# Optimization experiments

Measured on AMD Instinct MI355X. Metric: run time of the kernel, lower is better.

Reference implementation:

```python
import jax, jax.numpy as jnp
import numpy as np

N, E, D_IN, D_OUT = 50000, 800000, 128, 128
LN_EPS = 1e-5


def setup_inputs() -> dict:
    key = jax.random.key(0)
    ks = jax.random.split(key, 7)
    x = jax.random.normal(ks[0], (N, D_IN), dtype=jnp.float32)
    adj = jax.random.randint(ks[1], (2, E), 0, N, dtype=jnp.int32)  # edge_index
    scale = 1.0 / np.sqrt(D_IN)
    W_gcn = jax.random.normal(ks[2], (D_IN, D_OUT), dtype=jnp.float32) * scale
    b_gcn = jax.random.normal(ks[3], (D_OUT,), dtype=jnp.float32) * 0.02
    W_lin = jax.random.normal(ks[4], (D_IN, D_OUT), dtype=jnp.float32) * scale
    ln_w = jnp.ones((D_OUT,), dtype=jnp.float32)
    ln_b = jnp.zeros((D_OUT,), dtype=jnp.float32)
    return {"adj": adj, "x": x, "W_gcn": W_gcn, "b_gcn": b_gcn,
            "W_lin": W_lin, "ln_w": ln_w, "ln_b": ln_b}


def _gcn_conv(x, edge_index, W, b):
    """PyG GCNConv: add self-loops, symmetric D^-1/2 (A+I) D^-1/2 normalization."""
    n = x.shape[0]
    loop = jnp.arange(n, dtype=edge_index.dtype)
    src = jnp.concatenate([edge_index[0], loop])  # message sources (x_j)
    dst = jnp.concatenate([edge_index[1], loop])  # aggregation targets
    ones = jnp.ones(src.shape[0], dtype=x.dtype)
    deg = jax.ops.segment_sum(ones, dst, num_segments=n)
    dinv = jnp.where(deg > 0, jax.lax.rsqrt(deg), 0.0)
    norm = dinv[src] * dinv[dst]                   # [E+N]
    h = x @ W                                      # [N, D_OUT] project first (PyG order)
    msg = h[src] * norm[:, None]                   # gather + scale
    agg = jax.ops.segment_sum(msg, dst, num_segments=n)
    return agg + b


def _layer_norm(y, w, b):
    mu = jnp.mean(y, axis=-1, keepdims=True)
    var = jnp.mean(jnp.square(y - mu), axis=-1, keepdims=True)
    return (y - mu) * jax.lax.rsqrt(var + LN_EPS) * w + b


def reference(adj, x, W_gcn, b_gcn, W_lin, ln_w, ln_b):
    x1 = _gcn_conv(x, adj, W_gcn, b_gcn)
    x2 = x @ W_lin                                  # bias=False linear
    return _layer_norm(x1 + x2 + 1e-6, ln_w, ln_b)
```

## Files before the change

kernel.cpp:

```cpp
#include <hip/hip_runtime.h>
#include <hip/hip_bf16.h>

#define NN 50000
#define EE 800000
#define DD 128
#define CB 196
#define NFB 1563
#define EBLK 2048
#define NEBK 391
#define HST 392

typedef __attribute__((ext_vector_type(8))) short bf16x8;
typedef __attribute__((ext_vector_type(4))) float f32x4;

static __device__ __forceinline__ unsigned short f2bf(float f) {
  union { float f; unsigned u; } v; v.f = f;
  unsigned r = v.u + 0x7FFFu + ((v.u >> 16) & 1u);
  return (unsigned short)(r >> 16);
}
static __device__ __forceinline__ float bf2f(unsigned short h) {
  union { unsigned u; float f; } v; v.u = ((unsigned)h) << 16;
  return v.f;
}

__global__ __launch_bounds__(256) void k_p0(
    const int* __restrict__ dst, int* __restrict__ hist,
    const float* __restrict__ Wg, const float* __restrict__ Wl,
    unsigned short* __restrict__ Wt, const float4* __restrict__ x4,
    ushort4* __restrict__ xb4) {
  int b = blockIdx.x, t = threadIdx.x;
  if (b < NEBK) {
    __shared__ int cnt[CB];
    for (int i = t; i < CB; i += 256) cnt[i] = 0;
    __syncthreads();
    int e0 = b * EBLK;
    for (int i = t; i < EBLK; i += 256) {
      int e = e0 + i;
      if (e < EE) atomicAdd(&cnt[dst[e] >> 8], 1);
    }
    __syncthreads();
    if (t < CB) {
      hist[t * HST + b] = cnt[t];
      if (b == 0) hist[t * HST + (HST - 1)] = 0;
    }
  } else if (b < NEBK + 32) {
    for (int i = (b - NEBK) * 256 + t; i < DD * 256; i += 32 * 256) {
      int n = i >> 8, k = i & 255;
      float v = (k < 128) ? Wg[k * DD + n] : Wl[(k - 128) * DD + n];
      Wt[i] = f2bf(v);
    }
  } else {
    int base = (b - NEBK - 32) * 1024 + t;
#pragma unroll
    for (int k = 0; k < 4; k++) {
      int i = base + k * 256;
      if (i < NN * 32) {
        float4 v = x4[i];
        ushort4 o;
        o.x = f2bf(v.x); o.y = f2bf(v.y); o.z = f2bf(v.z); o.w = f2bf(v.w);
        xb4[i] = o;
      }
    }
  }
}

__global__ __launch_bounds__(512) void k_scatter(
    const int* __restrict__ src, const int* __restrict__ dst,
    const int* __restrict__ hist, int* __restrict__ bucketBase,
    int* __restrict__ bucketTot, unsigned int* __restrict__ pairs) {
  __shared__ unsigned int rec[EBLK];
  __shared__ unsigned int sorted[EBLK];
  __shared__ int sTo[2][CB], sCh[2][CB], sOw[2][CB];
  __shared__ unsigned int sc[256];
  __shared__ int cur[CB], gofs[CB];
  int blk = blockIdx.x, t = threadIdx.x;
  int e0 = blk * EBLK;
  int vcnt = EE - e0; if (vcnt > EBLK) vcnt = EBLK;
  for (int i = t; i < vcnt; i += 512) {
    int d = dst[e0 + i], s = src[e0 + i];
    rec[i] = (unsigned int)s | ((unsigned int)(d & 255) << 16) |
             ((unsigned int)(d >> 8) << 24);
  }
  int q = t & 255, h = t >> 8;
  if (q < CB) {
    const uint4* hp = (const uint4*)(hist + (size_t)q * HST + h * (HST / 2));
    int cb0 = h * (HST / 2);
    int to = 0, ch = 0, ow = 0;
#pragma unroll 7
    for (int v = 0; v < HST / 8; ++v) {
      uint4 hv = hp[v];
      int c = cb0 + v * 4;
      int a0 = (int)hv.x, a1 = (int)hv.y, a2 = (int)hv.z, a3 = (int)hv.w;
      to += a0 + a1 + a2 + a3;
      ch += (c + 0 < blk ? a0 : 0) + (c + 1 < blk ? a1 : 0) +
            (c + 2 < blk ? a2 : 0) + (c + 3 < blk ? a3 : 0);
      ow += (c + 0 == blk ? a0 : 0) + (c + 1 == blk ? a1 : 0) +
            (c + 2 == blk ? a2 : 0) + (c + 3 == blk ? a3 : 0);
    }
    sTo[h][q] = to; sCh[h][q] = ch; sOw[h][q] = ow;
  }
  __syncthreads();
  int totv = 0, chpv = 0, ownv = 0;
  if (t < CB) {
    totv = sTo[0][t] + sTo[1][t];
    chpv = sCh[0][t] + sCh[1][t];
    ownv = sOw[0][t] + sOw[1][t];
  }
  if (t < 256) sc[t] = (t < CB) ? (((unsigned)totv << 12) | (unsigned)ownv) : 0u;
  for (int off = 1; off < 256; off <<= 1) {
    __syncthreads();
    unsigned tmp = (t < 256 && t >= off) ? sc[t - off] : 0u;
    __syncthreads();
    if (t < 256 && t >= off) sc[t] += tmp;
  }
  __syncthreads();
  if (t < CB) {
    unsigned v = sc[t];
    int incT = (int)(v >> 12), incO = (int)(v & 4095u);
    int gb = incT - totv;
    int lo = incO - ownv;
    cur[t] = lo;
    gofs[t] = gb + chpv - lo;
    if (blk == 0) { bucketBase[t] = gb; bucketTot[t] = totv; }
  }
  __syncthreads();
  for (int i = t; i < vcnt; i += 512) {
    unsigned int r = rec[i];
    int p = atomicAdd(&cur[r >> 24], 1);
    sorted[p] = r;
  }
  __syncthreads();
  for (int i = t; i < vcnt; i += 512) {
    unsigned int r = sorted[i];
    pairs[gofs[r >> 24] + i] = r;
  }
}

__global__ __launch_bounds__(512) void k_p1b(
    const unsigned int* __restrict__ pairs, const int* __restrict__ bucketBase,
    const int* __restrict__ bucketTot, const unsigned short* __restrict__ xb,
    int* __restrict__ deg, float* __restrict__ dinv, int* __restrict__ rowStart,
    unsigned short* __restrict__ srcU16, unsigned short* __restrict__ xs) {
  __shared__ int ldeg[256], lscan[256], lcur[256];
  __shared__ float ldinvs[256];
  int b = blockIdx.x, t = threadIdx.x;
  int n0 = b << 8;
  int nloc = NN - n0; if (nloc > 256) nloc = 256;
  int start = bucketBase[b];
  int cnt = bucketTot[b];
  if (t < 256) ldeg[t] = 0;
  __syncthreads();
  for (int i = t; i < cnt; i += 512)
    atomicAdd(&ldeg[(pairs[start + i] >> 16) & 255], 1);
  __syncthreads();
  int dg = (t < 256) ? ldeg[t] : 0;
  if (t < 256) lscan[t] = dg;
  for (int off = 1; off < 256; off <<= 1) {
    __syncthreads();
    int tmp = (t < 256 && t >= off) ? lscan[t - off] : 0;
    __syncthreads();
    if (t < 256 && t >= off) lscan[t] += tmp;
  }
  __syncthreads();
  if (t < 256) {
    int rs = start + lscan[t] - dg;
    lcur[t] = rs;
    float di = rsqrtf((float)(dg + 1));
    ldinvs[t] = di;
    if (t < nloc) { deg[n0 + t] = dg; dinv[n0 + t] = di; rowStart[n0 + t] = rs; }
  }
  __syncthreads();
  for (int i = t; i < cnt; i += 512) {
    unsigned int pr = pairs[start + i];
    int pos = atomicAdd(&lcur[(pr >> 16) & 255], 1);
    srcU16[pos] = (unsigned short)(pr & 0xFFFFu);
  }
  for (int i = t; i < nloc * 16; i += 512) {
    int rr = i >> 4, qq = i & 15;
    bf16x8 v = *(const bf16x8*)(xb + (size_t)(n0 + rr) * DD + qq * 8);
    float di = ldinvs[rr];
    bf16x8 o;
#pragma unroll
    for (int k = 0; k < 8; k++) o[k] = (short)f2bf(bf2f((unsigned short)v[k]) * di);
    *(bf16x8*)(xs + (size_t)(n0 + rr) * DD + qq * 8) = o;
  }
}

static __device__ __forceinline__ void gather16(
    const unsigned short* __restrict__ xs, const unsigned short* __restrict__ srcU16,
    int js, int cnt, int r, int srcLaneBase, float* acc) {
  for (int base = 0; base < cnt; base += 16) {
    int idx = (base + r < cnt) ? (int)srcU16[js + base + r] : 0;
    int m = cnt - base; if (m > 16) m = 16;
    int j = 0;
    for (; j + 8 <= m; j += 8) {
      int s0 = __shfl(idx, srcLaneBase + j);
      int s1 = __shfl(idx, srcLaneBase + j + 1);
      int s2 = __shfl(idx, srcLaneBase + j + 2);
      int s3 = __shfl(idx, srcLaneBase + j + 3);
      int s4 = __shfl(idx, srcLaneBase + j + 4);
      int s5 = __shfl(idx, srcLaneBase + j + 5);
      int s6 = __shfl(idx, srcLaneBase + j + 6);
      int s7 = __shfl(idx, srcLaneBase + j + 7);
      bf16x8 v0 = *(const bf16x8*)(xs + (size_t)s0 * DD + r * 8);
      bf16x8 v1 = *(const bf16x8*)(xs + (size_t)s1 * DD + r * 8);
      bf16x8 v2 = *(const bf16x8*)(xs + (size_t)s2 * DD + r * 8);
      bf16x8 v3 = *(const bf16x8*)(xs + (size_t)s3 * DD + r * 8);
      bf16x8 v4 = *(const bf16x8*)(xs + (size_t)s4 * DD + r * 8);
      bf16x8 v5 = *(const bf16x8*)(xs + (size_t)s5 * DD + r * 8);
      bf16x8 v6 = *(const bf16x8*)(xs + (size_t)s6 * DD + r * 8);
      bf16x8 v7 = *(const bf16x8*)(xs + (size_t)s7 * DD + r * 8);
#pragma unroll
      for (int k = 0; k < 8; k++) acc[k] += bf2f((unsigned short)v0[k]);
#pragma unroll
      for (int k = 0; k < 8; k++) acc[k] += bf2f((unsigned short)v1[k]);
#pragma unroll
      for (int k = 0; k < 8; k++) acc[k] += bf2f((unsigned short)v2[k]);
#pragma unroll
      for (int k = 0; k < 8; k++) acc[k] += bf2f((unsigned short)v3[k]);
#pragma unroll
      for (int k = 0; k < 8; k++) acc[k] += bf2f((unsigned short)v4[k]);
#pragma unroll
      for (int k = 0; k < 8; k++) acc[k] += bf2f((unsigned short)v5[k]);
#pragma unroll
      for (int k = 0; k < 8; k++) acc[k] += bf2f((unsigned short)v6[k]);
#pragma unroll
      for (int k = 0; k < 8; k++) acc[k] += bf2f((unsigned short)v7[k]);
    }
    for (; j < m; j++) {
      int s = __shfl(idx, srcLaneBase + j);
      bf16x8 v = *(const bf16x8*)(xs + (size_t)s * DD + r * 8);
#pragma unroll
      for (int k = 0; k < 8; k++) acc[k] += bf2f((unsigned short)v[k]);
    }
  }
}

__global__ __launch_bounds__(512) void k_mega4(
    const unsigned short* __restrict__ xs, const unsigned short* __restrict__ xb,
    const int* __restrict__ rowStart, const int* __restrict__ deg,
    const unsigned short* __restrict__ srcU16, const float* __restrict__ dinv,
    const unsigned short* __restrict__ Wt, const float* __restrict__ bgcn,
    const float* __restrict__ lnw, const float* __restrict__ lnb,
    float* __restrict__ out) {
  __shared__ unsigned short abuf[32 * 136];
  int b = blockIdx.x, t = threadIdx.x;
  int n0 = b * 32;
  int g = t >> 4, r = t & 15;
  int lane = t & 63;
  int srcLaneBase = lane & 48;
  int node = n0 + g;
  bool valid = (node < NN);
  int nc = valid ? node : (NN - 1);
  float acc[8];
  {
    bf16x8 va = *(const bf16x8*)(xs + (size_t)nc * DD + r * 8);
#pragma unroll
    for (int k = 0; k < 8; k++) acc[k] = bf2f((unsigned short)va[k]);
  }
  int js = valid ? rowStart[nc] : 0;
  int cnt = valid ? deg[nc] : 0;
  gather16(xs, srcU16, js, cnt, r, srcLaneBase, acc);
  {
    float d = dinv[nc];
    bf16x8 o;
#pragma unroll
    for (int k = 0; k < 8; k++) o[k] = valid ? (short)f2bf(acc[k] * d) : (short)0;
    *(bf16x8*)&abuf[g * 136 + r * 8] = o;
  }
  __syncthreads();
  if (t < 128) {
    int w = t >> 6, lane2 = t & 63;
    int quad = lane2 >> 4, rr = lane2 & 15;
    int mloc = w * 16 + rr;
    int rowA = n0 + mloc; int rc = (rowA < NN) ? rowA : (NN - 1);
    f32x4 zero = {0.f, 0.f, 0.f, 0.f};
    f32x4 macc[8];
#pragma unroll
    for (int i = 0; i < 8; i++) macc[i] = zero;
#pragma unroll
    for (int ks = 0; ks < 8; ks++) {
      bf16x8 a;
      if (ks < 4) a = *(const bf16x8*)&abuf[mloc * 136 + ks * 32 + quad * 8];
      else        a = *(const bf16x8*)(xb + (size_t)rc * DD + (ks - 4) * 32 + quad * 8);
#pragma unroll
      for (int nt = 0; nt < 8; nt++) {
        bf16x8 bb = *(const bf16x8*)(Wt + (size_t)(nt * 16 + rr) * 256 + ks * 32 + quad * 8);
        macc[nt] = __builtin_amdgcn_mfma_f32_16x16x32_bf16(a, bb, macc[nt], 0, 0, 0);
      }
    }
    float bg[8], lw[8], lb[8];
#pragma unroll
    for (int nt = 0; nt < 8; nt++) {
      int col = nt * 16 + rr;
      bg[nt] = bgcn[col] + 1e-6f;
      lw[nt] = lnw[col];
      lb[nt] = lnb[col];
    }
#pragma unroll
    for (int reg = 0; reg < 4; reg++) {
      float y[8];
      float s1 = 0.f, s2 = 0.f;
#pragma unroll
      for (int nt = 0; nt < 8; nt++) {
        y[nt] = macc[nt][reg] + bg[nt];
        s1 += y[nt];
        s2 += y[nt] * y[nt];
      }
#pragma unroll
      for (int off = 1; off < 16; off <<= 1) {
        s1 += __shfl_xor(s1, off);
        s2 += __shfl_xor(s2, off);
      }
      float mu = s1 * (1.0f / 128.0f);
      float var = s2 * (1.0f / 128.0f) - mu * mu;
      float inv = rsqrtf(var + 1e-5f);
      int row = n0 + w * 16 + quad * 4 + reg;
      if (row < NN) {
#pragma unroll
        for (int nt = 0; nt < 8; nt++) {
          out[(size_t)row * DD + nt * 16 + rr] = (y[nt] - mu) * inv * lw[nt] + lb[nt];
        }
      }
    }
  }
}

extern "C" void kernel_launch(void* const* d_in, const int* in_sizes, int n_in,
                              void* d_out, int out_size, void* d_ws, size_t ws_size,
                              hipStream_t stream) {
  const int* adj = (const int*)d_in[0];
  const float* x = (const float*)d_in[1];
  const float* Wg = (const float*)d_in[2];
  const float* bg = (const float*)d_in[3];
  const float* Wl = (const float*)d_in[4];
  const float* lw = (const float*)d_in[5];
  const float* lb = (const float*)d_in[6];
  const int* srcp = adj;
  const int* dstp = adj + EE;
  float* out = (float*)d_out;

  char* ws = (char*)d_ws;
  size_t off = 0;
  auto alloc = [&](size_t bytes) -> void* {
    void* p = ws + off;
    off += (bytes + 255) & ~(size_t)255;
    return p;
  };
  int* hist = (int*)alloc((size_t)CB * HST * 4);
  int* bucketBase = (int*)alloc((size_t)256 * 4);
  int* bucketTot = (int*)alloc((size_t)256 * 4);
  unsigned int* pairs = (unsigned int*)alloc((size_t)EE * 4);
  unsigned short* srcU16 = (unsigned short*)alloc((size_t)EE * 2);
  int* deg = (int*)alloc((size_t)NN * 4);
  float* dinv = (float*)alloc((size_t)NN * 4);
  int* rowStart = (int*)alloc((size_t)NN * 4);
  unsigned short* xb = (unsigned short*)alloc((size_t)NN * DD * 2);
  unsigned short* xs = (unsigned short*)alloc((size_t)NN * DD * 2);
  unsigned short* Wt = (unsigned short*)alloc((size_t)DD * 256 * 2);
  (void)ws_size; (void)in_sizes; (void)n_in; (void)out_size;

  k_p0<<<NEBK + 32 + 1563, 256, 0, stream>>>(dstp, hist, Wg, Wl, Wt,
                                             (const float4*)x, (ushort4*)xb);
  k_scatter<<<NEBK, 512, 0, stream>>>(srcp, dstp, hist, bucketBase, bucketTot,
                                      pairs);
  k_p1b<<<CB, 512, 0, stream>>>(pairs, bucketBase, bucketTot, xb, deg, dinv,
                                rowStart, srcU16, xs);
  k_mega4<<<NFB, 512, 0, stream>>>(xs, xb, rowStart, deg, srcU16, dinv, Wt,
                                   bg, lw, lb, out);
}
```

Baseline: 187.1 us.

## Fuse preprocessing kernels into one cooperative kernel with grid syncs

Replaces the histogram, scatter and CSR-build kernels with a single cooperative kernel of 256 blocks that uses grid.sync between phases, and changes edge chunks from 2048 to 3125 per block. The aim is to remove two kernel launch boundaries and their tail effects. The scaled-x conversion now runs over the whole grid instead of only the 196 bucket blocks. In exchange, only 256 blocks are in flight during the bandwidth-bound x conversion, and each grid barrier adds its own cost.

```diff
diff --git a/kernel.cpp b/kernel.cpp
--- a/kernel.cpp
+++ b/kernel.cpp
@@ -1,4 +1,5 @@
 #include <hip/hip_runtime.h>
+#include <hip/hip_cooperative_groups.h>
 #include <hip/hip_bf16.h>
 
 #define NN 50000
@@ -6,12 +7,14 @@
 #define DD 128
 #define CB 196
 #define NFB 1563
-#define EBLK 2048
-#define NEBK 391
-#define HST 392
+#define GB 256
+#define GT 512
+#define ECH 3125
 
 typedef __attribute__((ext_vector_type(8))) short bf16x8;
 typedef __attribute__((ext_vector_type(4))) float f32x4;
+
+namespace cg = cooperative_groups;
 
 static __device__ __forceinline__ unsigned short f2bf(float f) {
   union { float f; unsigned u; } v; v.f = f;
@@ -23,88 +26,86 @@
   return v.f;
 }
 
-__global__ __launch_bounds__(256) void k_p0(
-    const int* __restrict__ dst, int* __restrict__ hist,
-    const float* __restrict__ Wg, const float* __restrict__ Wl,
-    unsigned short* __restrict__ Wt, const float4* __restrict__ x4,
-    ushort4* __restrict__ xb4) {
-  int b = blockIdx.x, t = threadIdx.x;
-  if (b < NEBK) {
-    __shared__ int cnt[CB];
-    for (int i = t; i < CB; i += 256) cnt[i] = 0;
-    __syncthreads();
-    int e0 = b * EBLK;
-    for (int i = t; i < EBLK; i += 256) {
-      int e = e0 + i;
-      if (e < EE) atomicAdd(&cnt[dst[e] >> 8], 1);
-    }
-    __syncthreads();
-    if (t < CB) {
-      hist[t * HST + b] = cnt[t];
-      if (b == 0) hist[t * HST + (HST - 1)] = 0;
-    }
-  } else if (b < NEBK + 32) {
-    for (int i = (b - NEBK) * 256 + t; i < DD * 256; i += 32 * 256) {
+__global__ __launch_bounds__(GT) void k_fused(
+    const int* __restrict__ src, const int* __restrict__ dst,
+    const float* __restrict__ x, const float* __restrict__ Wg,
+    const float* __restrict__ Wl, int* __restrict__ hist,
+    int* __restrict__ bucketBase, int* __restrict__ bucketTot,
+    unsigned int* __restrict__ pairs, unsigned short* __restrict__ srcU16,
+    int* __restrict__ deg, float* __restrict__ dinv,
+    int* __restrict__ rowStart, unsigned short* __restrict__ Wt,
+    unsigned short* __restrict__ xb, unsigned short* __restrict__ xs) {
+  __shared__ unsigned int smem[8320];
+  cg::grid_group grid = cg::this_grid();
+  int blk = blockIdx.x, t = threadIdx.x;
+
+  unsigned int* rec = smem;
+  int* cnt = (int*)(smem + 6272);
+  for (int i = t; i < CB; i += GT) cnt[i] = 0;
+  __syncthreads();
+  int e0 = blk * ECH;
+  for (int i = t; i < ECH; i += GT) {
+    int d = dst[e0 + i], s = src[e0 + i];
+    rec[i] = (unsigned)s | ((unsigned)(d & 255) << 16) |
+             ((unsigned)(d >> 8) << 24);
+    atomicAdd(&cnt[d >> 8], 1);
+  }
+  {
+    int i = blk * GT + t;
+    if (i < DD * 256) {
       int n = i >> 8, k = i & 255;
       float v = (k < 128) ? Wg[k * DD + n] : Wl[(k - 128) * DD + n];
       Wt[i] = f2bf(v);
     }
-  } else {
-    int base = (b - NEBK - 32) * 1024 + t;
-#pragma unroll
-    for (int k = 0; k < 4; k++) {
-      int i = base + k * 256;
-      if (i < NN * 32) {
-        float4 v = x4[i];
-        ushort4 o;
-        o.x = f2bf(v.x); o.y = f2bf(v.y); o.z = f2bf(v.z); o.w = f2bf(v.w);
-        xb4[i] = o;
-      }
-    }
-  }
-}
-
-__global__ __launch_bounds__(512) void k_scatter(
-    const int* __restrict__ src, const int* __restrict__ dst,
-    const int* __restrict__ hist, int* __restrict__ bucketBase,
-    int* __restrict__ bucketTot, unsigned int* __restrict__ pairs) {
-  __shared__ unsigned int rec[EBLK];
-  __shared__ unsigned int sorted[EBLK];
-  __shared__ int sTo[2][CB], sCh[2][CB], sOw[2][CB];
-  __shared__ unsigned int sc[256];
-  __shared__ int cur[CB], gofs[CB];
-  int blk = blockIdx.x, t = threadIdx.x;
-  int e0 = blk * EBLK;
-  int vcnt = EE - e0; if (vcnt > EBLK) vcnt = EBLK;
-  for (int i = t; i < vcnt; i += 512) {
-    int d = dst[e0 + i], s = src[e0 + i];
-    rec[i] = (unsigned int)s | ((unsigned int)(d & 255) << 16) |
-             ((unsigned int)(d >> 8) << 24);
-  }
-  int q = t & 255, h = t >> 8;
-  if (q < CB) {
-    const uint4* hp = (const uint4*)(hist + (size_t)q * HST + h * (HST / 2));
-    int cb0 = h * (HST / 2);
-    int to = 0, ch = 0, ow = 0;
-#pragma unroll 7
-    for (int v = 0; v < HST / 8; ++v) {
-      uint4 hv = hp[v];
-      int c = cb0 + v * 4;
-      int a0 = (int)hv.x, a1 = (int)hv.y, a2 = (int)hv.z, a3 = (int)hv.w;
-      to += a0 + a1 + a2 + a3;
-      ch += (c + 0 < blk ? a0 : 0) + (c + 1 < blk ? a1 : 0) +
-            (c + 2 < blk ? a2 : 0) + (c + 3 < blk ? a3 : 0);
-      ow += (c + 0 == blk ? a0 : 0) + (c + 1 == blk ? a1 : 0) +
-            (c + 2 == blk ? a2 : 0) + (c + 3 == blk ? a3 : 0);
-    }
-    sTo[h][q] = to; sCh[h][q] = ch; sOw[h][q] = ow;
+  }
+  {
+    const float4* x4 = (const float4*)x;
+    ushort4* xb4 = (ushort4*)xb;
+    for (int i = blk * GT + t; i < NN * 32; i += GB * GT) {
+      float4 v = x4[i];
+      ushort4 o;
+      o.x = f2bf(v.x); o.y = f2bf(v.y); o.z = f2bf(v.z); o.w = f2bf(v.w);
+      xb4[i] = o;
+    }
+  }
+  __syncthreads();
+  for (int i = t; i < CB; i += GT) hist[i * GB + blk] = cnt[i];
+  __threadfence();
+  grid.sync();
+
+  unsigned int* sorted = smem + 3136;
+  int* sTo = (int*)(smem + 6272);
+  int* sCh = (int*)(smem + 6664);
+  int* sOw = (int*)(smem + 7056);
+  unsigned int* sc = smem + 7448;
+  int* cur = (int*)(smem + 7704);
+  int* gofs = (int*)(smem + 7900);
+  {
+    int q = t & 255, h = t >> 8;
+    if (q < CB) {
+      const uint4* hp = (const uint4*)(hist + q * GB + h * 128);
+      int c0 = h * 128;
+      int to = 0, ch = 0, ow = 0;
+#pragma unroll 8
+      for (int v = 0; v < 32; ++v) {
+        uint4 hv = hp[v];
+        int c = c0 + v * 4;
+        int a0 = (int)hv.x, a1 = (int)hv.y, a2 = (int)hv.z, a3 = (int)hv.w;
+        to += a0 + a1 + a2 + a3;
+        ch += (c + 0 < blk ? a0 : 0) + (c + 1 < blk ? a1 : 0) +
+              (c + 2 < blk ? a2 : 0) + (c + 3 < blk ? a3 : 0);
+        ow += (c + 0 == blk ? a0 : 0) + (c + 1 == blk ? a1 : 0) +
+              (c + 2 == blk ? a2 : 0) + (c + 3 == blk ? a3 : 0);
+      }
+      sTo[h * CB + q] = to; sCh[h * CB + q] = ch; sOw[h * CB + q] = ow;
+    }
   }
   __syncthreads();
   int totv = 0, chpv = 0, ownv = 0;
   if (t < CB) {
-    totv = sTo[0][t] + sTo[1][t];
-    chpv = sCh[0][t] + sCh[1][t];
-    ownv = sOw[0][t] + sOw[1][t];
+    totv = sTo[t] + sTo[CB + t];
+    chpv = sCh[t] + sCh[CB + t];
+    ownv = sOw[t] + sOw[CB + t];
   }
   if (t < 256) sc[t] = (t < CB) ? (((unsigned)totv << 12) | (unsigned)ownv) : 0u;
   for (int off = 1; off < 256; off <<= 1) {
@@ -116,73 +117,74 @@
   __syncthreads();
   if (t < CB) {
     unsigned v = sc[t];
-    int incT = (int)(v >> 12), incO = (int)(v & 4095u);
-    int gb = incT - totv;
-    int lo = incO - ownv;
+    int gb = (int)(v >> 12) - totv;
+    int lo = (int)(v & 4095u) - ownv;
     cur[t] = lo;
     gofs[t] = gb + chpv - lo;
     if (blk == 0) { bucketBase[t] = gb; bucketTot[t] = totv; }
   }
   __syncthreads();
-  for (int i = t; i < vcnt; i += 512) {
-    unsigned int r = rec[i];
+  for (int i = t; i < ECH; i += GT) {
+    unsigned r = rec[i];
     int p = atomicAdd(&cur[r >> 24], 1);
     sorted[p] = r;
   }
   __syncthreads();
-  for (int i = t; i < vcnt; i += 512) {
-    unsigned int r = sorted[i];
+  for (int i = t; i < ECH; i += GT) {
+    unsigned r = sorted[i];
     pairs[gofs[r >> 24] + i] = r;
   }
-}
-
-__global__ __launch_bounds__(512) void k_p1b(
-    const unsigned int* __restrict__ pairs, const int* __restrict__ bucketBase,
-    const int* __restrict__ bucketTot, const unsigned short* __restrict__ xb,
-    int* __restrict__ deg, float* __restrict__ dinv, int* __restrict__ rowStart,
-    unsigned short* __restrict__ srcU16, unsigned short* __restrict__ xs) {
-  __shared__ int ldeg[256], lscan[256], lcur[256];
-  __shared__ float ldinvs[256];
-  int b = blockIdx.x, t = threadIdx.x;
-  int n0 = b << 8;
-  int nloc = NN - n0; if (nloc > 256) nloc = 256;
-  int start = bucketBase[b];
-  int cnt = bucketTot[b];
-  if (t < 256) ldeg[t] = 0;
-  __syncthreads();
-  for (int i = t; i < cnt; i += 512)
-    atomicAdd(&ldeg[(pairs[start + i] >> 16) & 255], 1);
-  __syncthreads();
-  int dg = (t < 256) ? ldeg[t] : 0;
-  if (t < 256) lscan[t] = dg;
-  for (int off = 1; off < 256; off <<= 1) {
-    __syncthreads();
-    int tmp = (t < 256 && t >= off) ? lscan[t - off] : 0;
-    __syncthreads();
-    if (t < 256 && t >= off) lscan[t] += tmp;
-  }
-  __syncthreads();
-  if (t < 256) {
-    int rs = start + lscan[t] - dg;
-    lcur[t] = rs;
-    float di = rsqrtf((float)(dg + 1));
-    ldinvs[t] = di;
-    if (t < nloc) { deg[n0 + t] = dg; dinv[n0 + t] = di; rowStart[n0 + t] = rs; }
-  }
-  __syncthreads();
-  for (int i = t; i < cnt; i += 512) {
-    unsigned int pr = pairs[start + i];
-    int pos = atomicAdd(&lcur[(pr >> 16) & 255], 1);
-    srcU16[pos] = (unsigned short)(pr & 0xFFFFu);
-  }
-  for (int i = t; i < nloc * 16; i += 512) {
-    int rr = i >> 4, qq = i & 15;
-    bf16x8 v = *(const bf16x8*)(xb + (size_t)(n0 + rr) * DD + qq * 8);
-    float di = ldinvs[rr];
+  __threadfence();
+  grid.sync();
+
+  int* ldeg = (int*)smem;
+  int* lscan = (int*)smem + 256;
+  int* lcur = (int*)smem + 512;
+  if (blk < CB) {
+    int n0 = blk << 8;
+    int nloc = NN - n0; if (nloc > 256) nloc = 256;
+    int start = bucketBase[blk], cntb = bucketTot[blk];
+    if (t < 256) ldeg[t] = 0;
+    __syncthreads();
+    for (int i = t; i < cntb; i += GT)
+      atomicAdd(&ldeg[(pairs[start + i] >> 16) & 255], 1);
+    __syncthreads();
+    int dg = (t < 256) ? ldeg[t] : 0;
+    if (t < 256) lscan[t] = dg;
+    for (int off = 1; off < 256; off <<= 1) {
+      __syncthreads();
+      int tmp = (t < 256 && t >= off) ? lscan[t - off] : 0;
+      __syncthreads();
+      if (t < 256 && t >= off) lscan[t] += tmp;
+    }
+    __syncthreads();
+    if (t < 256) {
+      int rs = start + lscan[t] - dg;
+      lcur[t] = rs;
+      if (t < nloc) {
+        deg[n0 + t] = dg;
+        dinv[n0 + t] = rsqrtf((float)(dg + 1));
+        rowStart[n0 + t] = rs;
+      }
+    }
+    __syncthreads();
+    for (int i = t; i < cntb; i += GT) {
+      unsigned pr = pairs[start + i];
+      int pos = atomicAdd(&lcur[(pr >> 16) & 255], 1);
+      srcU16[pos] = (unsigned short)(pr & 0xFFFFu);
+    }
+  }
+  __threadfence();
+  grid.sync();
+
+  for (int i = blk * GT + t; i < NN * 16; i += GB * GT) {
+    int row = i >> 4;
+    float di = dinv[row];
+    bf16x8 v = *(const bf16x8*)(xb + (size_t)i * 8);
     bf16x8 o;
 #pragma unroll
     for (int k = 0; k < 8; k++) o[k] = (short)f2bf(bf2f((unsigned short)v[k]) * di);
-    *(bf16x8*)(xs + (size_t)(n0 + rr) * DD + qq * 8) = o;
+    *(bf16x8*)(xs + (size_t)i * 8) = o;
   }
 }
 
@@ -347,7 +349,7 @@
     off += (bytes + 255) & ~(size_t)255;
     return p;
   };
-  int* hist = (int*)alloc((size_t)CB * HST * 4);
+  int* hist = (int*)alloc((size_t)CB * GB * 4);
   int* bucketBase = (int*)alloc((size_t)256 * 4);
   int* bucketTot = (int*)alloc((size_t)256 * 4);
   unsigned int* pairs = (unsigned int*)alloc((size_t)EE * 4);
@@ -360,12 +362,13 @@
   unsigned short* Wt = (unsigned short*)alloc((size_t)DD * 256 * 2);
   (void)ws_size; (void)in_sizes; (void)n_in; (void)out_size;
 
-  k_p0<<<NEBK + 32 + 1563, 256, 0, stream>>>(dstp, hist, Wg, Wl, Wt,
-                                             (const float4*)x, (ushort4*)xb);
-  k_scatter<<<NEBK, 512, 0, stream>>>(srcp, dstp, hist, bucketBase, bucketTot,
-                                      pairs);
-  k_p1b<<<CB, 512, 0, stream>>>(pairs, bucketBase, bucketTot, xb, deg, dinv,
-                                rowStart, srcU16, xs);
+  void* args[] = {(void*)&srcp, (void*)&dstp, (void*)&x, (void*)&Wg,
+                  (void*)&Wl, (void*)&hist, (void*)&bucketBase,
+                  (void*)&bucketTot, (void*)&pairs, (void*)&srcU16,
+                  (void*)&deg, (void*)&dinv, (void*)&rowStart, (void*)&Wt,
+                  (void*)&xb, (void*)&xs};
+  hipLaunchCooperativeKernel((const void*)k_fused, dim3(GB), dim3(GT), args, 0,
+                             stream);
   k_mega4<<<NFB, 512, 0, stream>>>(xs, xb, rowStart, deg, srcU16, dinv, Wt,
                                    bg, lw, lb, out);
 }
```

Result: slower. 422.7 us (+125.9%).

## Split fused GEMM+LayerNorm epilogue across all 8 waves with LDS row-stat reduction

Applied to the files above, without the earlier changes.

Previously only 2 of 8 waves ran the MFMA GEMM and LayerNorm epilogue while the other 6 sat idle. Now every wave computes a 16-row by 32-column tile, so the per-wave MFMA chain and register use shrink. Row sums for LayerNorm are combined across the four column-pair waves through shared memory. This costs an extra barrier and more total loads of A from LDS and xb.

```diff
diff --git a/kernel.cpp b/kernel.cpp
--- a/kernel.cpp
+++ b/kernel.cpp
@@ -236,7 +236,7 @@
   }
 }
 
-__global__ __launch_bounds__(512) void k_mega4(
+__global__ __launch_bounds__(512) void k_mega5(
     const unsigned short* __restrict__ xs, const unsigned short* __restrict__ xb,
     const int* __restrict__ rowStart, const int* __restrict__ deg,
     const unsigned short* __restrict__ srcU16, const float* __restrict__ dinv,
@@ -244,6 +244,7 @@
     const float* __restrict__ lnw, const float* __restrict__ lnb,
     float* __restrict__ out) {
   __shared__ unsigned short abuf[32 * 136];
+  __shared__ float lnred[4][32][2];
   int b = blockIdx.x, t = threadIdx.x;
   int n0 = b * 32;
   int g = t >> 4, r = t & 15;
@@ -269,58 +270,68 @@
     *(bf16x8*)&abuf[g * 136 + r * 8] = o;
   }
   __syncthreads();
-  if (t < 128) {
-    int w = t >> 6, lane2 = t & 63;
-    int quad = lane2 >> 4, rr = lane2 & 15;
-    int mloc = w * 16 + rr;
-    int rowA = n0 + mloc; int rc = (rowA < NN) ? rowA : (NN - 1);
-    f32x4 zero = {0.f, 0.f, 0.f, 0.f};
-    f32x4 macc[8];
-#pragma unroll
-    for (int i = 0; i < 8; i++) macc[i] = zero;
-#pragma unroll
-    for (int ks = 0; ks < 8; ks++) {
-      bf16x8 a;
-      if (ks < 4) a = *(const bf16x8*)&abuf[mloc * 136 + ks * 32 + quad * 8];
-      else        a = *(const bf16x8*)(xb + (size_t)rc * DD + (ks - 4) * 32 + quad * 8);
-#pragma unroll
-      for (int nt = 0; nt < 8; nt++) {
-        bf16x8 bb = *(const bf16x8*)(Wt + (size_t)(nt * 16 + rr) * 256 + ks * 32 + quad * 8);
-        macc[nt] = __builtin_amdgcn_mfma_f32_16x16x32_bf16(a, bb, macc[nt], 0, 0, 0);
-      }
-    }
-    float bg[8], lw[8], lb[8];
-#pragma unroll
-    for (int nt = 0; nt < 8; nt++) {
-      int col = nt * 16 + rr;
-      bg[nt] = bgcn[col] + 1e-6f;
-      lw[nt] = lnw[col];
-      lb[nt] = lnb[col];
-    }
-#pragma unroll
-    for (int reg = 0; reg < 4; reg++) {
-      float y[8];
-      float s1 = 0.f, s2 = 0.f;
-#pragma unroll
-      for (int nt = 0; nt < 8; nt++) {
-        y[nt] = macc[nt][reg] + bg[nt];
-        s1 += y[nt];
-        s2 += y[nt] * y[nt];
-      }
-#pragma unroll
-      for (int off = 1; off < 16; off <<= 1) {
-        s1 += __shfl_xor(s1, off);
-        s2 += __shfl_xor(s2, off);
-      }
-      float mu = s1 * (1.0f / 128.0f);
-      float var = s2 * (1.0f / 128.0f) - mu * mu;
-      float inv = rsqrtf(var + 1e-5f);
-      int row = n0 + w * 16 + quad * 4 + reg;
-      if (row < NN) {
-#pragma unroll
-        for (int nt = 0; nt < 8; nt++) {
-          out[(size_t)row * DD + nt * 16 + rr] = (y[nt] - mu) * inv * lw[nt] + lb[nt];
-        }
+  int w = t >> 6, lane2 = t & 63;
+  int quad = lane2 >> 4, rr = lane2 & 15;
+  int rowTile = w & 1, colPair = w >> 1;
+  int mloc = rowTile * 16 + rr;
+  int rowA = n0 + mloc; int rc = (rowA < NN) ? rowA : (NN - 1);
+  f32x4 zero = {0.f, 0.f, 0.f, 0.f};
+  f32x4 macc[2];
+  macc[0] = zero; macc[1] = zero;
+#pragma unroll
+  for (int ks = 0; ks < 8; ks++) {
+    bf16x8 a;
+    if (ks < 4) a = *(const bf16x8*)&abuf[mloc * 136 + ks * 32 + quad * 8];
+    else        a = *(const bf16x8*)(xb + (size_t)rc * DD + (ks - 4) * 32 + quad * 8);
+#pragma unroll
+    for (int j = 0; j < 2; j++) {
+      int nt = colPair * 2 + j;
+      bf16x8 bb = *(const bf16x8*)(Wt + (size_t)(nt * 16 + rr) * 256 + ks * 32 + quad * 8);
+      macc[j] = __builtin_amdgcn_mfma_f32_16x16x32_bf16(a, bb, macc[j], 0, 0, 0);
+    }
+  }
+  float bg[2], lw[2], lb[2];
+#pragma unroll
+  for (int j = 0; j < 2; j++) {
+    int col = (colPair * 2 + j) * 16 + rr;
+    bg[j] = bgcn[col] + 1e-6f;
+    lw[j] = lnw[col];
+    lb[j] = lnb[col];
+  }
+#pragma unroll
+  for (int reg = 0; reg < 4; reg++) {
+    float y0 = macc[0][reg] + bg[0];
+    float y1 = macc[1][reg] + bg[1];
+    float s1 = y0 + y1, s2 = y0 * y0 + y1 * y1;
+#pragma unroll
+    for (int off = 1; off < 16; off <<= 1) {
+      s1 += __shfl_xor(s1, off);
+      s2 += __shfl_xor(s2, off);
+    }
+    if (rr == 0) {
+      int rloc = rowTile * 16 + quad * 4 + reg;
+      lnred[colPair][rloc][0] = s1;
+      lnred[colPair][rloc][1] = s2;
+    }
+  }
+  __syncthreads();
+#pragma unroll
+  for (int reg = 0; reg < 4; reg++) {
+    int rloc = rowTile * 16 + quad * 4 + reg;
+    float s1 = lnred[0][rloc][0] + lnred[1][rloc][0] +
+               lnred[2][rloc][0] + lnred[3][rloc][0];
+    float s2 = lnred[0][rloc][1] + lnred[1][rloc][1] +
+               lnred[2][rloc][1] + lnred[3][rloc][1];
+    float mu = s1 * (1.0f / 128.0f);
+    float var = s2 * (1.0f / 128.0f) - mu * mu;
+    float inv = rsqrtf(var + 1e-5f);
+    int row = n0 + rloc;
+    if (row < NN) {
+#pragma unroll
+      for (int j = 0; j < 2; j++) {
+        float y = macc[j][reg] + bg[j];
+        out[(size_t)row * DD + (colPair * 2 + j) * 16 + rr] =
+            (y - mu) * inv * lw[j] + lb[j];
       }
     }
   }
@@ -366,6 +377,6 @@
                                       pairs);
   k_p1b<<<CB, 512, 0, stream>>>(pairs, bucketBase, bucketTot, xb, deg, dinv,
                                 rowStart, srcU16, xs);
-  k_mega4<<<NFB, 512, 0, stream>>>(xs, xb, rowStart, deg, srcU16, dinv, Wt,
+  k_mega5<<<NFB, 512, 0, stream>>>(xs, xb, rowStart, deg, srcU16, dinv, Wt,
                                    bg, lw, lb, out);
 }
```

Measured after the change: 189.0 us. About the same (+1.0%).
